# Kernel tuning notes

Hardware: AMD Instinct MI355X
Metric: run time of the kernel (lower is better)

## Reference

```python
import jax, jax.numpy as jnp
import numpy as np

K_MASK = -2.3819763e+38
B, T, D = 2, 2048, 2048
N, K, H = 8, 2, 256          # query heads, kv heads, head dim
F = 8192                     # ffn hidden
A = 4                        # num_altup_inputs
P = 4                        # num_modalities
WINDOW = 512
SOFT_CAP = 50.0
Q_SCALE = H ** -0.5
ROPE_BASE = 10000.0


def rms_norm(x, scale=None, eps=1e-6):
    y = x * jax.lax.rsqrt(jnp.mean(jnp.square(x), axis=-1, keepdims=True) + eps)
    if scale is not None:
        y = y * (1.0 + scale)   # scale_plus_one=True
    return y


def apply_rope(x, pos, base=ROPE_BASE, scale_factor=1.0):
    # x: [B,T,num_heads,H], pos: [B,T]
    h = x.shape[-1]
    frac = 2.0 * jnp.arange(h // 2, dtype=jnp.float32) / h
    timescale = base ** frac
    sin_inp = (pos[..., None].astype(jnp.float32) / timescale)[..., None, :] / scale_factor  # [B,T,1,H/2]
    sin, cos = jnp.sin(sin_inp), jnp.cos(sin_inp)
    x1, x2 = jnp.split(x, 2, axis=-1)
    return jnp.concatenate([x1 * cos - x2 * sin, x2 * cos + x1 * sin], axis=-1).astype(x.dtype)


def setup_inputs():
    key = jax.random.key(0)
    ks = jax.random.split(key, 12)
    r = lambda i, shape, s=0.02: jax.random.normal(ks[i], shape, dtype=jnp.float32) * s
    pos = jnp.broadcast_to(jnp.arange(T, dtype=jnp.int32), (B, T))
    causal = pos[:, :, None] >= pos[:, None, :]  # [B,T,T] bool
    return dict(
        x=jax.random.normal(ks[0], (A, B, T, D), dtype=jnp.float32),
        segment_pos=pos,
        attn_mask=causal,
        router_w=r(1, (D, P), 1.0),
        pred_coefs=r(2, (P, A, A), 0.0001),
        corr_coefs=r(3, (P, A), 0.01),
        correct_output_scale=jnp.ones((D,), jnp.float32),
        pre_attn_scale=jnp.zeros((D,), jnp.float32),
        q_w=r(4, (N, D, H)),
        kv_w=r(5, (2, K, D, H)),
        qk_q_scale=jnp.zeros((H,), jnp.float32),
        qk_k_scale=jnp.zeros((H,), jnp.float32),
        o_w=r(6, (N, H, D)),
        post_attn_scale=jnp.zeros((D,), jnp.float32),
        pre_ffw_scale=jnp.zeros((D,), jnp.float32),
        gate_w=r(7, (D, F)),
        up_w=r(8, (D, F)),
        down_w=r(9, (F, D)),
        post_ffw_scale=jnp.zeros((D,), jnp.float32),
    )


def _router(h, router_w):
    # modality router: scale by 1/d_model, project, tanh in fp32
    return jnp.tanh(jnp.einsum('btd,dp->btp', h * (1.0 / D), router_w).astype(jnp.float32))


def _attention(x, segment_pos, attn_mask, q_w, kv_w, qk_q_scale, qk_k_scale, o_w):
    q = jnp.einsum('btd,ndh->btnh', x, q_w)               # [B,T,N,H]
    k, v = jnp.einsum('bsd,ckdh->cbskh', x, kv_w)         # each [B,T,K,H]
    q = rms_norm(q, qk_q_scale)                           # qk norm
    k = rms_norm(k, qk_k_scale)
    v = rms_norm(v)                                       # value norm (no scale)
    q = apply_rope(q, segment_pos) * Q_SCALE
    k = apply_rope(k, segment_pos)
    g = N // K                                            # GQA group size
    qr = q.reshape(B, T, K, g, H)
    logits = jnp.einsum('btkgh,bskh->btkgs', qr, k).reshape(B, T, N, T)
    logits = jnp.tanh(logits / SOFT_CAP) * SOFT_CAP       # attn_logits_soft_cap
    # sliding-window mask combined with causal attn_mask
    sliding = (segment_pos[:, None, :] > segment_pos[:, :, None] - WINDOW) & \
              (segment_pos[:, None, :] < segment_pos[:, :, None] + WINDOW)
    mask = attn_mask & sliding
    padded = jnp.where(mask[:, :, None, :], logits, K_MASK)
    probs = jax.nn.softmax(padded, axis=-1).astype(k.dtype)
    enc = jnp.einsum('btkgs,bskh->btkgh', probs.reshape(B, T, K, g, T), v).reshape(B, T, N, H)
    return jnp.einsum('btnh,nhd->btd', enc, o_w)


def reference(x, segment_pos, attn_mask, router_w, pred_coefs, corr_coefs,
              correct_output_scale, pre_attn_scale, q_w, kv_w, qk_q_scale, qk_k_scale,
              o_w, post_attn_scale, pre_ffw_scale, gate_w, up_w, down_w, post_ffw_scale):
    # ---- AltUp predict ----
    mods = _router(x[0], router_w)                                   # [B,T,P]
    coefs = jnp.einsum('btp,pij->btij', mods, pred_coefs.astype(jnp.float32))
    predictions = x + jnp.einsum('btij,jbtd->ibtd', coefs, x).astype(x.dtype)
    active = predictions[0]
    # ---- attention block ----
    attn_in = rms_norm(active, pre_attn_scale)
    attn = _attention(attn_in, segment_pos, attn_mask, q_w, kv_w, qk_q_scale, qk_k_scale, o_w)
    attn = rms_norm(attn, post_attn_scale)
    attn_gated = active + attn
    # ---- gated-GELU MLP ----
    h = rms_norm(attn_gated, pre_ffw_scale)
    ffw = jnp.einsum('btf,fd->btd', jax.nn.gelu(h @ gate_w) * (h @ up_w), down_w)
    ffw = rms_norm(ffw, post_ffw_scale)
    activated = attn_gated + ffw
    # ---- AltUp correct (with scale_corrected_output) ----
    activated = activated * correct_output_scale
    mods_c = _router(activated, router_w)
    c = jnp.einsum('btp,pi->bti', mods_c, corr_coefs.astype(jnp.float32)) + 1.0
    innovation = activated - predictions[0]
    corrected = predictions + jnp.einsum('bti,btd->ibtd', c, innovation).astype(x.dtype)
    return corrected
```

## Files before the change

kernel.cpp:

```cpp
#include <hip/hip_runtime.h>
#include <hip/hip_bf16.h>

typedef unsigned short u16;
typedef __attribute__((ext_vector_type(8))) short bf16x8_t;
typedef __attribute__((ext_vector_type(4))) float f32x4_t;

#define DEV __device__ __forceinline__

constexpr int cB = 2, cT = 2048, cD = 2048;
constexpr int cN = 8, cK = 2, cH = 256, cF = 8192;
constexpr int cBT = cB * cT;
constexpr float cEPS = 1e-6f;
constexpr float cQS = 0.0625f;
constexpr float cCAP = 50.0f;
constexpr int cWIN = 512;
constexpr int cNH = 12;

DEV u16 f2bf(float f) {
  union { float f; unsigned u; } c; c.f = f;
  unsigned u = c.u;
  return (u16)((u + 0x7fffu + ((u >> 16) & 1u)) >> 16);
}
DEV float bf2f(u16 h) {
  union { unsigned u; float f; } c; c.u = ((unsigned)h) << 16;
  return c.f;
}
DEV float g4(const float4& v, int k) { return k == 0 ? v.x : k == 1 ? v.y : k == 2 ? v.z : v.w; }
DEV void store_bf4(u16* p, float a, float b, float c, float d) {
  union { u16 h[4]; uint2 v; } o;
  o.h[0] = f2bf(a); o.h[1] = f2bf(b); o.h[2] = f2bf(c); o.h[3] = f2bf(d);
  *(uint2*)p = o.v;
}
DEV float tanh_fast(float x) {
  float e2 = __expf(2.0f * x);
  return 1.0f - 2.0f * __builtin_amdgcn_rcpf(e2 + 1.0f);
}
DEV float gelu_fast(float x) {
  float u = 1.5957691216057308f * (x + 0.044715f * x * x * x);
  float e2 = __expf(u);
  return x * (1.0f - __builtin_amdgcn_rcpf(e2 + 1.0f));
}

DEV float block_sum256(float v, float* sbuf) {
  #pragma unroll
  for (int m = 32; m > 0; m >>= 1) v += __shfl_xor(v, m, 64);
  int wid = threadIdx.x >> 6;
  if ((threadIdx.x & 63) == 0) sbuf[wid] = v;
  __syncthreads();
  float tot = sbuf[0] + sbuf[1] + sbuf[2] + sbuf[3];
  __syncthreads();
  return tot;
}
DEV void block_sum256x4(float v[4], float* sbuf ) {
  #pragma unroll
  for (int m = 32; m > 0; m >>= 1) {
    #pragma unroll
    for (int k = 0; k < 4; k++) v[k] += __shfl_xor(v[k], m, 64);
  }
  int wid = threadIdx.x >> 6;
  if ((threadIdx.x & 63) == 0) *(float4*)(sbuf + wid * 4) = make_float4(v[0], v[1], v[2], v[3]);
  __syncthreads();
  #pragma unroll
  for (int k = 0; k < 4; k++) v[k] = sbuf[k] + sbuf[4 + k] + sbuf[8 + k] + sbuf[12 + k];
  __syncthreads();
}

#define GLD_LDS16(gp, lp) __builtin_amdgcn_global_load_lds( \
    (const __attribute__((address_space(1))) void*)(gp),    \
    (__attribute__((address_space(3))) void*)(lp), 16, 0, 0)

#define WAITV(n) asm volatile("s_waitcnt vmcnt(" #n ")" ::: "memory")
#define LGKM(n)  asm volatile("s_waitcnt lgkmcnt(" #n ")" ::: "memory")
#define SCHED0() __builtin_amdgcn_sched_barrier(0)
#define LDS_ADDR(p) ((unsigned)(uintptr_t)(__attribute__((address_space(3))) const void*)(p))
#define DSR(dst, base, off) \
  asm volatile("ds_read_b128 %0, %1 offset:" off : "=v"(dst) : "v"(base))

__global__ __launch_bounds__(256) void k_transpose_cast(
    const float* __restrict__ src, u16* __restrict__ dst, int R, int C, int gu) {
  __shared__ float tile[64][65];
  size_t base = (size_t)blockIdx.z * R * C;
  int c0 = blockIdx.x * 64, r0 = blockIdx.y * 64;
  int tx = threadIdx.x & 15, ty = threadIdx.x >> 4;
  #pragma unroll
  for (int i = 0; i < 4; i++) {
    int r = ty + i * 16;
    float4 v = *(const float4*)(src + base + (size_t)(r0 + r) * C + c0 + tx * 4);
    tile[r][tx * 4 + 0] = v.x; tile[r][tx * 4 + 1] = v.y;
    tile[r][tx * 4 + 2] = v.z; tile[r][tx * 4 + 3] = v.w;
  }
  __syncthreads();
  #pragma unroll
  for (int i = 0; i < 4; i++) {
    int j = ty + i * 16;
    int c = c0 + j;
    int n = (gu < 0) ? c : (((c >> 4) << 5) + (gu << 4) + (c & 15));
    store_bf4(dst + base + (size_t)n * R + r0 + tx * 4,
              tile[tx * 4 + 0][j], tile[tx * 4 + 1][j],
              tile[tx * 4 + 2][j], tile[tx * 4 + 3][j]);
  }
}

__global__ __launch_bounds__(256) void k_rope_table(
    const int* __restrict__ pos, float2* __restrict__ rt) {
  int idx = blockIdx.x * 256 + threadIdx.x;
  int bt = idx >> 7, j = idx & 127;
  float p = (float)pos[bt];
  float ts = powf(10000.0f, (2.0f * j) * (1.0f / cH));
  float si = p / ts;
  rt[idx] = make_float2(sinf(si), cosf(si));
}

__global__ __launch_bounds__(256) void k_predict(
    const float* __restrict__ x, const float* __restrict__ router_w,
    const float* __restrict__ pred_coefs, const float* __restrict__ pre_attn_scale,
    float* __restrict__ out, u16* __restrict__ attn_in) {
  __shared__ float sbuf[16];
  int bt = blockIdx.x, tid = threadIdx.x;
  const size_t PL = (size_t)cBT * cD;
  const size_t rowb = (size_t)bt * cD;
  float4 xv[4][2];
  #pragma unroll
  for (int j = 0; j < 4; j++)
    #pragma unroll
    for (int u = 0; u < 2; u++)
      xv[j][u] = *(const float4*)(x + j * PL + rowb + (u * 256 + tid) * 4);
  float rp[4] = {0, 0, 0, 0};
  #pragma unroll
  for (int u = 0; u < 2; u++)
    #pragma unroll
    for (int k = 0; k < 4; k++) {
      int e = (u * 256 + tid) * 4 + k;
      float4 rw = *(const float4*)(router_w + (size_t)e * 4);
      float xe = g4(xv[0][u], k);
      rp[0] += xe * rw.x; rp[1] += xe * rw.y; rp[2] += xe * rw.z; rp[3] += xe * rw.w;
    }
  block_sum256x4(rp, sbuf);
  float mods[4];
  #pragma unroll
  for (int p = 0; p < 4; p++) mods[p] = tanh_fast(rp[p] * (1.0f / cD));
  float coef[4][4];
  #pragma unroll
  for (int i = 0; i < 4; i++)
    #pragma unroll
    for (int j = 0; j < 4; j++) {
      float s = 0;
      #pragma unroll
      for (int p = 0; p < 4; p++) s += mods[p] * pred_coefs[(p * 4 + i) * 4 + j];
      coef[i][j] = s;
    }
  float4 p04[2]; float ssq = 0;
  #pragma unroll
  for (int u = 0; u < 2; u++)
    #pragma unroll
    for (int i = 0; i < 4; i++) {
      float4 s = xv[i][u];
      #pragma unroll
      for (int j = 0; j < 4; j++) {
        s.x += coef[i][j] * xv[j][u].x; s.y += coef[i][j] * xv[j][u].y;
        s.z += coef[i][j] * xv[j][u].z; s.w += coef[i][j] * xv[j][u].w;
      }
      *(float4*)(out + i * PL + rowb + (u * 256 + tid) * 4) = s;
      if (i == 0) { p04[u] = s; ssq += s.x * s.x + s.y * s.y + s.z * s.z + s.w * s.w; }
    }
  float rs = rsqrtf(block_sum256(ssq, sbuf) * (1.0f / cD) + cEPS);
  #pragma unroll
  for (int u = 0; u < 2; u++) {
    int e0 = (u * 256 + tid) * 4;
    float4 sc = *(const float4*)(pre_attn_scale + e0);
    store_bf4(attn_in + rowb + e0,
              p04[u].x * rs * (1.0f + sc.x), p04[u].y * rs * (1.0f + sc.y),
              p04[u].z * rs * (1.0f + sc.z), p04[u].w * rs * (1.0f + sc.w));
  }
}

template <int OUT_MODE>
__global__ __launch_bounds__(512, 2) void k_gemm8p(
    const u16* __restrict__ A, const u16* __restrict__ Bt, void* __restrict__ Cv,
    int Nn, int Kk) {
  constexpr int MI = 8;
  constexpr int A_KS = 256 * 32;
  constexpr int B_KS = 256 * 32;
  constexpr int BUF_E = 2 * A_KS + 2 * B_KS;
  extern __shared__ u16 lds[];

  const int tid = threadIdx.x;
  const int wid = tid >> 6, lane = tid & 63;
  const int wr = wid >> 2, wc = wid & 3;
  const int fr = lane & 15, fq = lane >> 4;

  const int nwg = gridDim.x * gridDim.y;
  const int flat = blockIdx.y * gridDim.x + blockIdx.x;
  const int swz = (flat & 7) * (nwg >> 3) + (flat >> 3);
  const int m0 = (swz % gridDim.x) * 256;
  const int n0 = (swz / gridDim.x) * 256;
  const int NT = Kk >> 6;
  const int NH = NT * 2;

  const int srow = lane >> 2, sslot = lane & 3;
  const int scol = (sslot ^ ((srow >> 1) & 3)) * 8;
  const u16* aSrc0 = A + (size_t)(m0 + wid * 16 + srow) * Kk + scol;
  const u16* aSrc1 = A + (size_t)(m0 + 128 + wid * 16 + srow) * Kk + scol;
  const u16* bSrc0 = Bt + (size_t)(n0 + wid * 16 + srow) * Kk + scol;
  const u16* bSrc1 = Bt + (size_t)(n0 + 128 + wid * 16 + srow) * Kk + scol;

  const int swzR = (fq ^ ((fr >> 1) & 3)) * 8;
  const unsigned base0 = LDS_ADDR(lds);
  const unsigned aoffB = (unsigned)(((wr * 128 + fr) * 32 + swzR) * 2);
  const unsigned boffB = (unsigned)((2 * A_KS + (wc * 64 + fr) * 32 + swzR) * 2);
  const unsigned aB0 = base0 + aoffB, aB1 = base0 + BUF_E * 2 + aoffB;
  const unsigned bB0 = base0 + boffB, bB1 = base0 + BUF_E * 2 + boffB;

  auto stageH = [&](int h) {
    int tt = h >> 1, ks = h & 1;
    int koff = h * 32;
    u16* dstA = lds + (tt & 1) * BUF_E + ks * A_KS + wid * 512;
    GLD_LDS16(aSrc0 + koff, dstA);
    GLD_LDS16(aSrc1 + koff, dstA + 128 * 32);
    u16* dstB = lds + (tt & 1) * BUF_E + 2 * A_KS + ks * B_KS + wid * 512;
    GLD_LDS16(bSrc0 + koff, dstB);
    GLD_LDS16(bSrc1 + koff, dstB + 128 * 32);
  };

  f32x4_t acc[MI][4];
  #pragma unroll
  for (int i = 0; i < MI; i++)
    #pragma unroll
    for (int j = 0; j < 4; j++) acc[i][j] = (f32x4_t){0.f, 0.f, 0.f, 0.f};

  bf16x8_t aX[8], aY[8], bX[4], bY[4];

#define READS_KS0(ab, bb, av, bv) do {                                   \
    DSR(av[0], ab, "0");     DSR(av[1], ab, "1024");                     \
    DSR(av[2], ab, "2048");  DSR(av[3], ab, "3072");                     \
    DSR(av[4], ab, "4096");  DSR(av[5], ab, "5120");                     \
    DSR(av[6], ab, "6144");  DSR(av[7], ab, "7168");                     \
    DSR(bv[0], bb, "0");     DSR(bv[1], bb, "1024");                     \
    DSR(bv[2], bb, "2048");  DSR(bv[3], bb, "3072");  } while (0)
#define READS_KS1(ab, bb, av, bv) do {                                   \
    DSR(av[0], ab, "16384"); DSR(av[1], ab, "17408");                    \
    DSR(av[2], ab, "18432"); DSR(av[3], ab, "19456");                    \
    DSR(av[4], ab, "20480"); DSR(av[5], ab, "21504");                    \
    DSR(av[6], ab, "22528"); DSR(av[7], ab, "23552");                    \
    DSR(bv[0], bb, "16384"); DSR(bv[1], bb, "17408");                    \
    DSR(bv[2], bb, "18432"); DSR(bv[3], bb, "19456"); } while (0)

#define MFMA32(av, bv)                                                    \
  __builtin_amdgcn_s_setprio(1);                                          \
  _Pragma("unroll")                                                       \
  for (int i = 0; i < 8; i++) {                                           \
    acc[i][0] = __builtin_amdgcn_mfma_f32_16x16x32_bf16(av[i], bv[0], acc[i][0], 0, 0, 0); \
    acc[i][1] = __builtin_amdgcn_mfma_f32_16x16x32_bf16(av[i], bv[1], acc[i][1], 0, 0, 0); \
    acc[i][2] = __builtin_amdgcn_mfma_f32_16x16x32_bf16(av[i], bv[2], acc[i][2], 0, 0, 0); \
    acc[i][3] = __builtin_amdgcn_mfma_f32_16x16x32_bf16(av[i], bv[3], acc[i][3], 0, 0, 0); \
  }                                                                       \
  __builtin_amdgcn_s_setprio(0);

  stageH(0); asm volatile("" ::: "memory");
  stageH(1); asm volatile("" ::: "memory");
  stageH(2);
  WAITV(8);
  __builtin_amdgcn_s_barrier();
  SCHED0();
  READS_KS0(aB0, bB0, aX, bX);

  for (int t = 0; t < NT; t++) {
    const unsigned aPb = (t & 1) ? aB1 : aB0;
    const unsigned bPb = (t & 1) ? bB1 : bB0;
    const unsigned aNb = (t & 1) ? aB0 : aB1;
    const unsigned bNb = (t & 1) ? bB0 : bB1;

    {
      const int R = NH - 1 - 2 * t;
      if (R >= 2) WAITV(4); else WAITV(0);
      __builtin_amdgcn_s_barrier();
      SCHED0();
      if (R >= 3) stageH(2 * t + 3);
      READS_KS1(aPb, bPb, aY, bY);
      LGKM(12);
      SCHED0();
      MFMA32(aX, bX)
    }
    {
      const int R = NH - 2 - 2 * t;
      if (R >= 2) WAITV(4); else if (R == 1) WAITV(0);
      __builtin_amdgcn_s_barrier();
      SCHED0();
      if (R >= 3) stageH(2 * t + 4);
      if (R >= 1) {
        READS_KS0(aNb, bNb, aX, bX);
        LGKM(12);
      } else {
        LGKM(0);
      }
      SCHED0();
      MFMA32(aY, bY)
    }
  }
#undef MFMA32
#undef READS_KS0
#undef READS_KS1

  if constexpr (OUT_MODE == 2) {
    const int Nh = Nn >> 1;
    #pragma unroll
    for (int i = 0; i < MI; i++)
      #pragma unroll
      for (int jp = 0; jp < 2; jp++) {
        int c = (n0 + wc * 64 + jp * 32) / 2 + fr;
        #pragma unroll
        for (int r = 0; r < 4; r++) {
          int m = m0 + wr * (MI * 16) + i * 16 + fq * 4 + r;
          float g = acc[i][2 * jp][r], uu = acc[i][2 * jp + 1][r];
          ((u16*)Cv)[(size_t)m * Nh + c] = f2bf(gelu_fast(g) * uu);
        }
      }
  } else {
    #pragma unroll
    for (int i = 0; i < MI; i++)
      #pragma unroll
      for (int j = 0; j < 4; j++)
        #pragma unroll
        for (int r = 0; r < 4; r++) {
          int m = m0 + wr * (MI * 16) + i * 16 + fq * 4 + r;
          int n = n0 + wc * 64 + j * 16 + fr;
          ((u16*)Cv)[(size_t)m * Nn + n] = f2bf(acc[i][j][r]);
        }
  }
}

template <int OUT_MODE>
__global__ __launch_bounds__(512, 2) void k_gemm4r(
    const u16* __restrict__ A, const u16* __restrict__ Bt, void* __restrict__ Cv,
    int Nn, int Kk) {
  constexpr int MI = 4;
  constexpr int BM = 128;
  constexpr int A_KS = BM * 32;
  constexpr int B_KS = 256 * 32;
  constexpr int SLOT_E = 2 * A_KS + 2 * B_KS;
  extern __shared__ u16 lds[];

  const int tid = threadIdx.x;
  const int wid = tid >> 6, lane = tid & 63;
  const int wr = wid >> 2, wc = wid & 3;
  const int fr = lane & 15, fq = lane >> 4;

  const int nwg = gridDim.x * gridDim.y;
  const int flat = blockIdx.y * gridDim.x + blockIdx.x;
  const int swz = (flat & 7) * (nwg >> 3) + (flat >> 3);
  const int m0 = (swz % gridDim.x) * BM;
  const int n0 = (swz / gridDim.x) * 256;
  const int NT = Kk >> 6;

  const int srow = lane >> 2, sslot = lane & 3;

  auto stageA = [&](int t, int ks) {
    u16* buf = lds + (t % 3) * SLOT_E + ks * A_KS;
    int row0 = wid * 16;
    int row = row0 + srow;
    int col = (sslot ^ ((row >> 1) & 3)) * 8;
    GLD_LDS16(A + (size_t)(m0 + row) * Kk + t * 64 + ks * 32 + col, buf + row0 * 32);
  };
  auto stageB = [&](int t, int ks) {
    u16* buf = lds + (t % 3) * SLOT_E + 2 * A_KS + ks * B_KS;
    #pragma unroll
    for (int i = 0; i < 2; i++) {
      int row0 = i * 128 + wid * 16;
      int row = row0 + srow;
      int col = (sslot ^ ((row >> 1) & 3)) * 8;
      GLD_LDS16(Bt + (size_t)(n0 + row) * Kk + t * 64 + ks * 32 + col, buf + row0 * 32);
    }
  };
  auto readA = [&](const u16* buf, int ks, int i) -> bf16x8_t {
    int row = wr * 64 + i * 16 + fr;
    return *(const bf16x8_t*)(buf + ks * A_KS + row * 32 + (fq ^ ((row >> 1) & 3)) * 8);
  };
  auto readB = [&](const u16* buf, int ks, int j) -> bf16x8_t {
    int row = wc * 64 + j * 16 + fr;
    return *(const bf16x8_t*)(buf + 2 * A_KS + ks * B_KS + row * 32 + (fq ^ ((row >> 1) & 3)) * 8);
  };

  f32x4_t acc[MI][4];
  #pragma unroll
  for (int i = 0; i < MI; i++)
    #pragma unroll
    for (int j = 0; j < 4; j++) acc[i][j] = (f32x4_t){0.f, 0.f, 0.f, 0.f};

  stageA(0, 0); stageB(0, 0); stageA(0, 1); stageB(0, 1);
  stageA(1, 0); stageB(1, 0); stageA(1, 1); stageB(1, 1);
  WAITV(9);
  __builtin_amdgcn_s_barrier();

#define PHASE_MFMA4(J0)                                                             \
  __builtin_amdgcn_s_setprio(1);                                                    \
  _Pragma("unroll")                                                                 \
  for (int i = 0; i < MI; i++) {                                                    \
    acc[i][J0]     = __builtin_amdgcn_mfma_f32_16x16x32_bf16(a0[i], b0[0], acc[i][J0], 0, 0, 0);     \
    acc[i][J0 + 1] = __builtin_amdgcn_mfma_f32_16x16x32_bf16(a0[i], b0[1], acc[i][J0 + 1], 0, 0, 0); \
  }                                                                                 \
  __builtin_amdgcn_s_setprio(0);

  for (int t = 0; t < NT; t++) {
    const u16* buf = lds + (t % 3) * SLOT_E;
    const bool pf2 = (t + 2 < NT);
    const bool pf1 = (t + 1 < NT);
    bf16x8_t a0[MI], b0[2];

    #pragma unroll
    for (int i = 0; i < MI; i++) a0[i] = readA(buf, 0, i);
    b0[0] = readB(buf, 0, 0); b0[1] = readB(buf, 0, 1);
    if (pf2) stageA(t + 2, 0);
    __builtin_amdgcn_s_barrier();
    PHASE_MFMA4(0)
    __builtin_amdgcn_s_barrier();

    b0[0] = readB(buf, 0, 2); b0[1] = readB(buf, 0, 3);
    if (pf2) stageB(t + 2, 0);
    if (pf2) WAITV(9); else if (pf1) WAITV(6); else WAITV(0);
    __builtin_amdgcn_s_barrier();
    PHASE_MFMA4(2)
    __builtin_amdgcn_s_barrier();

    #pragma unroll
    for (int i = 0; i < MI; i++) a0[i] = readA(buf, 1, i);
    b0[0] = readB(buf, 1, 0); b0[1] = readB(buf, 1, 1);
    if (pf2) stageA(t + 2, 1);
    __builtin_amdgcn_s_barrier();
    PHASE_MFMA4(0)
    __builtin_amdgcn_s_barrier();

    b0[0] = readB(buf, 1, 2); b0[1] = readB(buf, 1, 3);
    if (pf2) stageB(t + 2, 1);
    if (pf2) WAITV(9); else if (pf1) WAITV(3);
    __builtin_amdgcn_s_barrier();
    PHASE_MFMA4(2)
    __builtin_amdgcn_s_barrier();
  }
#undef PHASE_MFMA4

  #pragma unroll
  for (int i = 0; i < MI; i++)
    #pragma unroll
    for (int j = 0; j < 4; j++)
      #pragma unroll
      for (int r = 0; r < 4; r++) {
        int m = m0 + wr * 64 + i * 16 + fq * 4 + r;
        int n = n0 + wc * 64 + j * 16 + fr;
        float v = acc[i][j][r];
        if (OUT_MODE == 1) ((u16*)Cv)[(size_t)m * Nn + n] = f2bf(v);
        else ((float*)Cv)[(size_t)m * Nn + n] = v;
      }
}

__global__ __launch_bounds__(64) void k_qkvpost(
    u16* __restrict__ qkv, const float* __restrict__ qscale,
    const float* __restrict__ kscale, const float2* __restrict__ rt,
    u16* __restrict__ vT) {
  int h = blockIdx.x % cNH, bt = blockIdx.x / cNH;
  int lane = threadIdx.x;
  u16* row = qkv + ((size_t)bt * cNH + h) * cH;
  float v[4], ssq = 0;
  #pragma unroll
  for (int m = 0; m < 4; m++) { v[m] = bf2f(row[lane + 64 * m]); ssq += v[m] * v[m]; }
  #pragma unroll
  for (int mm = 32; mm > 0; mm >>= 1) ssq += __shfl_xor(ssq, mm, 64);
  float rs = rsqrtf(ssq * (1.0f / cH) + cEPS);
  if (h < 10) {
    const float* sc = (h < 8) ? qscale : kscale;
    float os = (h < 8) ? cQS : 1.0f;
    #pragma unroll
    for (int m = 0; m < 4; m++) {
      int e = lane + 64 * m;
      v[m] = v[m] * rs * (1.0f + sc[e]);
    }
    #pragma unroll
    for (int m = 0; m < 2; m++) {
      int j = lane + 64 * m;
      float2 t = rt[bt * 128 + j];
      float x1 = v[m], x2 = v[m + 2];
      row[j]       = f2bf((x1 * t.y - x2 * t.x) * os);
      row[j + 128] = f2bf((x2 * t.y + x1 * t.x) * os);
    }
  } else {
    int kk = h - 10;
    int b = bt / cT, t = bt % cT;
    #pragma unroll
    for (int m = 0; m < 4; m++) {
      int e = lane + 64 * m;
      vT[((size_t)(b * cK + kk) * cH + e) * cT + t] = f2bf(v[m] * rs);
    }
  }
}

__global__ __launch_bounds__(64) void k_attn(
    const u16* __restrict__ qkv, const u16* __restrict__ vT, u16* __restrict__ enc) {
  int t0 = blockIdx.x * 16;
  int n = blockIdx.y, b = blockIdx.z;
  int kn = n >> 2;
  int lane = threadIdx.x;
  int fr = lane & 15, fq = lane >> 4;
  __shared__ float P[16][33];

  bf16x8_t qf[8];
  const u16* qrow = qkv + ((size_t)(b * cT + t0 + fr) * cNH + n) * cH;
  #pragma unroll
  for (int ks = 0; ks < 8; ks++) qf[ks] = *(const bf16x8_t*)(qrow + ks * 32 + fq * 8);

  f32x4_t acc[16];
  #pragma unroll
  for (int ht = 0; ht < 16; ht++) acc[ht] = (f32x4_t){0.f, 0.f, 0.f, 0.f};
  float psum[4] = {0.f, 0.f, 0.f, 0.f};

  int s_lo = t0 - (cWIN - 1); if (s_lo < 0) s_lo = 0; s_lo &= ~31;
  for (int s0 = s_lo; s0 <= t0 + 15; s0 += 32) {
    f32x4_t S[2];
    S[0] = (f32x4_t){0.f, 0.f, 0.f, 0.f};
    S[1] = (f32x4_t){0.f, 0.f, 0.f, 0.f};
    #pragma unroll
    for (int c = 0; c < 2; c++) {
      const u16* krow = qkv + ((size_t)(b * cT + s0 + c * 16 + fr) * cNH + 8 + kn) * cH;
      #pragma unroll
      for (int ks = 0; ks < 8; ks++) {
        bf16x8_t kf = *(const bf16x8_t*)(krow + ks * 32 + fq * 8);
        S[c] = __builtin_amdgcn_mfma_f32_16x16x32_bf16(qf[ks], kf, S[c], 0, 0, 0);
      }
    }
    #pragma unroll
    for (int c = 0; c < 2; c++) {
      int s = s0 + c * 16 + fr;
      #pragma unroll
      for (int r = 0; r < 4; r++) {
        int t = t0 + fq * 4 + r;
        float l = cCAP * tanh_fast(S[c][r] * (1.0f / cCAP));
        float pe = (s <= t && s >= t - (cWIN - 1)) ? __expf(l) : 0.0f;
        psum[r] += pe;
        P[fq * 4 + r][c * 16 + fr] = pe;
      }
    }
    bf16x8_t pf;
    #pragma unroll
    for (int e = 0; e < 8; e++) pf[e] = (short)f2bf(P[fr][fq * 8 + e]);
    #pragma unroll
    for (int ht = 0; ht < 16; ht++) {
      bf16x8_t vf = *(const bf16x8_t*)(vT + (((size_t)(b * cK + kn)) * cH + ht * 16 + fr) * cT + s0 + fq * 8);
      acc[ht] = __builtin_amdgcn_mfma_f32_16x16x32_bf16(pf, vf, acc[ht], 0, 0, 0);
    }
  }
  #pragma unroll
  for (int r = 0; r < 4; r++) {
    #pragma unroll
    for (int m = 1; m < 16; m <<= 1) psum[r] += __shfl_xor(psum[r], m, 64);
  }
  float inv[4];
  #pragma unroll
  for (int r = 0; r < 4; r++) inv[r] = 1.0f / psum[r];
  #pragma unroll
  for (int ht = 0; ht < 16; ht++)
    #pragma unroll
    for (int r = 0; r < 4; r++)
      enc[(((size_t)(b * cT + t0 + fq * 4 + r)) * cN + n) * cH + ht * 16 + fr] =
          f2bf(acc[ht][r] * inv[r]);
}

__global__ __launch_bounds__(256) void k_postattn(
    const float* __restrict__ attn_raw, const float* __restrict__ out0,
    const float* __restrict__ post_attn_scale, const float* __restrict__ pre_ffw_scale,
    float* __restrict__ ag, u16* __restrict__ h) {
  __shared__ float sbuf[4];
  int bt = blockIdx.x, tid = threadIdx.x;
  const size_t rowb = (size_t)bt * cD;
  float4 ar[2]; float ssq = 0;
  #pragma unroll
  for (int u = 0; u < 2; u++) {
    ar[u] = *(const float4*)(attn_raw + rowb + (u * 256 + tid) * 4);
    ssq += ar[u].x * ar[u].x + ar[u].y * ar[u].y + ar[u].z * ar[u].z + ar[u].w * ar[u].w;
  }
  float rs = rsqrtf(block_sum256(ssq, sbuf) * (1.0f / cD) + cEPS);
  float4 agv[2]; float ssq2 = 0;
  #pragma unroll
  for (int u = 0; u < 2; u++) {
    int e0 = (u * 256 + tid) * 4;
    float4 o0 = *(const float4*)(out0 + rowb + e0);
    float4 sc = *(const float4*)(post_attn_scale + e0);
    float4 a;
    a.x = o0.x + ar[u].x * rs * (1.0f + sc.x);
    a.y = o0.y + ar[u].y * rs * (1.0f + sc.y);
    a.z = o0.z + ar[u].z * rs * (1.0f + sc.z);
    a.w = o0.w + ar[u].w * rs * (1.0f + sc.w);
    agv[u] = a;
    *(float4*)(ag + rowb + e0) = a;
    ssq2 += a.x * a.x + a.y * a.y + a.z * a.z + a.w * a.w;
  }
  float rs2 = rsqrtf(block_sum256(ssq2, sbuf) * (1.0f / cD) + cEPS);
  #pragma unroll
  for (int u = 0; u < 2; u++) {
    int e0 = (u * 256 + tid) * 4;
    float4 sc = *(const float4*)(pre_ffw_scale + e0);
    store_bf4(h + rowb + e0,
              agv[u].x * rs2 * (1.0f + sc.x), agv[u].y * rs2 * (1.0f + sc.y),
              agv[u].z * rs2 * (1.0f + sc.z), agv[u].w * rs2 * (1.0f + sc.w));
  }
}

__global__ __launch_bounds__(256) void k_final(
    const float* __restrict__ ffw_raw, const float* __restrict__ ag,
    const float* __restrict__ post_ffw_scale, const float* __restrict__ cos_scale,
    const float* __restrict__ router_w, const float* __restrict__ corr_coefs,
    float* __restrict__ out) {
  __shared__ float sbuf[16];
  int bt = blockIdx.x, tid = threadIdx.x;
  const size_t PL = (size_t)cBT * cD;
  const size_t rowb = (size_t)bt * cD;
  float4 fv[2]; float ssq = 0;
  #pragma unroll
  for (int u = 0; u < 2; u++) {
    fv[u] = *(const float4*)(ffw_raw + rowb + (u * 256 + tid) * 4);
    ssq += fv[u].x * fv[u].x + fv[u].y * fv[u].y + fv[u].z * fv[u].z + fv[u].w * fv[u].w;
  }
  float rs = rsqrtf(block_sum256(ssq, sbuf) * (1.0f / cD) + cEPS);
  float4 av[2];
  float rp[4] = {0, 0, 0, 0};
  #pragma unroll
  for (int u = 0; u < 2; u++) {
    int e0 = (u * 256 + tid) * 4;
    float4 agx = *(const float4*)(ag + rowb + e0);
    float4 ps = *(const float4*)(post_ffw_scale + e0);
    float4 cs = *(const float4*)(cos_scale + e0);
    float4 a;
    a.x = (agx.x + fv[u].x * rs * (1.0f + ps.x)) * cs.x;
    a.y = (agx.y + fv[u].y * rs * (1.0f + ps.y)) * cs.y;
    a.z = (agx.z + fv[u].z * rs * (1.0f + ps.z)) * cs.z;
    a.w = (agx.w + fv[u].w * rs * (1.0f + ps.w)) * cs.w;
    av[u] = a;
    #pragma unroll
    for (int k = 0; k < 4; k++) {
      float4 rw = *(const float4*)(router_w + (size_t)(e0 + k) * 4);
      float xe = g4(a, k);
      rp[0] += xe * rw.x; rp[1] += xe * rw.y; rp[2] += xe * rw.z; rp[3] += xe * rw.w;
    }
  }
  block_sum256x4(rp, sbuf);
  float cc[4];
  #pragma unroll
  for (int i = 0; i < 4; i++) {
    float s = 1.0f;
    #pragma unroll
    for (int p = 0; p < 4; p++) s += tanh_fast(rp[p] * (1.0f / cD)) * corr_coefs[p * 4 + i];
    cc[i] = s;
  }
  #pragma unroll
  for (int u = 0; u < 2; u++) {
    size_t o = rowb + (u * 256 + tid) * 4;
    float4 p0 = *(const float4*)(out + o);
    float4 in4;
    in4.x = av[u].x - p0.x; in4.y = av[u].y - p0.y;
    in4.z = av[u].z - p0.z; in4.w = av[u].w - p0.w;
    float4 w0;
    w0.x = p0.x + cc[0] * in4.x; w0.y = p0.y + cc[0] * in4.y;
    w0.z = p0.z + cc[0] * in4.z; w0.w = p0.w + cc[0] * in4.w;
    *(float4*)(out + o) = w0;
    #pragma unroll
    for (int i = 1; i < 4; i++) {
      float4 q = *(const float4*)(out + i * PL + o);
      q.x += cc[i] * in4.x; q.y += cc[i] * in4.y;
      q.z += cc[i] * in4.z; q.w += cc[i] * in4.w;
      *(float4*)(out + i * PL + o) = q;
    }
  }
}

extern "C" void kernel_launch(void* const* d_in, const int* in_sizes, int n_in,
                              void* d_out, int out_size, void* d_ws, size_t ws_size,
                              hipStream_t stream) {
  const float* x              = (const float*)d_in[0];
  const int*   pos            = (const int*)d_in[1];
  const float* router_w       = (const float*)d_in[3];
  const float* pred_coefs     = (const float*)d_in[4];
  const float* corr_coefs     = (const float*)d_in[5];
  const float* cos_scale      = (const float*)d_in[6];
  const float* pre_attn_scale = (const float*)d_in[7];
  const float* q_w            = (const float*)d_in[8];
  const float* kv_w           = (const float*)d_in[9];
  const float* qk_q_scale     = (const float*)d_in[10];
  const float* qk_k_scale     = (const float*)d_in[11];
  const float* o_w            = (const float*)d_in[12];
  const float* post_attn_scale= (const float*)d_in[13];
  const float* pre_ffw_scale  = (const float*)d_in[14];
  const float* gate_w         = (const float*)d_in[15];
  const float* up_w           = (const float*)d_in[16];
  const float* down_w         = (const float*)d_in[17];
  const float* post_ffw_scale = (const float*)d_in[18];
  float* out = (float*)d_out;

  char* wsp = (char*)d_ws;
  size_t off = 0;
  auto take = [&](size_t nbytes) -> char* {
    char* p = wsp + off;
    off += (nbytes + 255) & ~((size_t)255);
    return p;
  };
  u16* gu_wT    = (u16*)take((size_t)2 * cF * cD * 2);
  u16* down_wT  = (u16*)take((size_t)cD * cF * 2);
  u16* qkv_wT   = (u16*)take((size_t)cNH * cH * cD * 2);
  u16* o_wT     = (u16*)take((size_t)cD * cN * cH * 2);
  u16* attn_in  = (u16*)take((size_t)cBT * cD * 2);
  u16* qkvbuf   = (u16*)take((size_t)cBT * cNH * cH * 2);
  u16* vTbuf    = (u16*)take((size_t)cB * cK * cH * cT * 2);
  u16* encbuf   = (u16*)take((size_t)cBT * cN * cH * 2);
  float* attn_raw = (float*)take((size_t)cBT * cD * 4);
  float* agbuf    = (float*)take((size_t)cBT * cD * 4);
  u16* hbuf     = (u16*)take((size_t)cBT * cD * 2);
  u16* Gcbuf    = (u16*)take((size_t)cBT * cF * 2);
  float* ffw_raw = (float*)take((size_t)cBT * cD * 4);
  float2* ropetab = (float2*)take((size_t)cBT * 128 * 8);
  (void)in_sizes; (void)n_in; (void)out_size; (void)ws_size;

  dim3 blk256(256), blk64(64), blk512(512);
  constexpr unsigned LDS8  = 2 * (2 * 256 * 32 + 2 * 256 * 32) * 2;
  constexpr unsigned LDS4R = 3 * (2 * 128 * 32 + 2 * 256 * 32) * 2;

  k_transpose_cast<<<dim3(cF / 64, cD / 64, 1), blk256, 0, stream>>>(gate_w, gu_wT, cD, cF, 0);
  k_transpose_cast<<<dim3(cF / 64, cD / 64, 1), blk256, 0, stream>>>(up_w, gu_wT, cD, cF, 1);
  k_transpose_cast<<<dim3(cD / 64, cF / 64, 1), blk256, 0, stream>>>(down_w, down_wT, cF, cD, -1);
  k_transpose_cast<<<dim3(cH / 64, cD / 64, cN), blk256, 0, stream>>>(q_w, qkv_wT, cD, cH, -1);
  k_transpose_cast<<<dim3(cH / 64, cD / 64, 2 * cK), blk256, 0, stream>>>(
      kv_w, qkv_wT + (size_t)cN * cH * cD, cD, cH, -1);
  k_transpose_cast<<<dim3(cD / 64, (cN * cH) / 64, 1), blk256, 0, stream>>>(o_w, o_wT, cN * cH, cD, -1);
  k_rope_table<<<dim3(cBT * 128 / 256), blk256, 0, stream>>>(pos, ropetab);

  k_predict<<<dim3(cBT), blk256, 0, stream>>>(x, router_w, pred_coefs, pre_attn_scale, out, attn_in);

  k_gemm4r<1><<<dim3(cBT / 128, (cNH * cH) / 256), blk512, LDS4R, stream>>>(
      attn_in, qkv_wT, qkvbuf, cNH * cH, cD);

  k_qkvpost<<<dim3(cBT * cNH), blk64, 0, stream>>>(qkvbuf, qk_q_scale, qk_k_scale, ropetab, vTbuf);

  k_attn<<<dim3(cT / 16, cN, cB), blk64, 0, stream>>>(qkvbuf, vTbuf, encbuf);

  k_gemm4r<0><<<dim3(cBT / 128, cD / 256), blk512, LDS4R, stream>>>(
      encbuf, o_wT, attn_raw, cD, cN * cH);
  k_postattn<<<dim3(cBT), blk256, 0, stream>>>(attn_raw, out, post_attn_scale, pre_ffw_scale, agbuf, hbuf);

  k_gemm8p<2><<<dim3(cBT / 256, (2 * cF) / 256), blk512, LDS8, stream>>>(
      hbuf, gu_wT, Gcbuf, 2 * cF, cD);
  k_gemm4r<0><<<dim3(cBT / 128, cD / 256), blk512, LDS4R, stream>>>(
      Gcbuf, down_wT, ffw_raw, cD, cF);

  k_final<<<dim3(cBT), blk256, 0, stream>>>(ffw_raw, agbuf, post_ffw_scale, cos_scale,
                                            router_w, corr_coefs, out);
}
```

Baseline: 950.5 us.

## Rewrite 128x256 GEMM main loop with double-buffered register prefetch and inline-asm LDS reads

Replaces the k_gemm4r main loop with a restructured k_gemm4p. It prefetches the next half-K slice of A/B fragments from LDS into a second register set (aX/aY, bX/bY) while MFMAs run on the current set. LDS reads now use precomputed byte addresses with immediate offsets via inline asm, and barriers per K-tile drop from eight to two. The aim is to hide LDS latency behind MFMA work and cut address arithmetic and synchronisation, at the cost of more VGPRs and reliance on hand-placed waitcnt and scheduling barriers.

```diff
diff --git a/kernel.cpp b/kernel.cpp
--- a/kernel.cpp
+++ b/kernel.cpp
@@ -330,14 +330,13 @@
 }
 
 template <int OUT_MODE>
-__global__ __launch_bounds__(512, 2) void k_gemm4r(
+__global__ __launch_bounds__(512, 2) void k_gemm4p(
     const u16* __restrict__ A, const u16* __restrict__ Bt, void* __restrict__ Cv,
     int Nn, int Kk) {
-  constexpr int MI = 4;
-  constexpr int BM = 128;
-  constexpr int A_KS = BM * 32;
+  constexpr int A_KS = 128 * 32;
   constexpr int B_KS = 256 * 32;
   constexpr int SLOT_E = 2 * A_KS + 2 * B_KS;
+  constexpr unsigned SLOT_B = 49152;
   extern __shared__ u16 lds[];
 
   const int tid = threadIdx.x;
@@ -348,98 +347,115 @@
   const int nwg = gridDim.x * gridDim.y;
   const int flat = blockIdx.y * gridDim.x + blockIdx.x;
   const int swz = (flat & 7) * (nwg >> 3) + (flat >> 3);
-  const int m0 = (swz % gridDim.x) * BM;
+  const int m0 = (swz % gridDim.x) * 128;
   const int n0 = (swz / gridDim.x) * 256;
   const int NT = Kk >> 6;
+  const int NH = NT * 2;
 
   const int srow = lane >> 2, sslot = lane & 3;
-
-  auto stageA = [&](int t, int ks) {
-    u16* buf = lds + (t % 3) * SLOT_E + ks * A_KS;
-    int row0 = wid * 16;
-    int row = row0 + srow;
-    int col = (sslot ^ ((row >> 1) & 3)) * 8;
-    GLD_LDS16(A + (size_t)(m0 + row) * Kk + t * 64 + ks * 32 + col, buf + row0 * 32);
+  const int scol = (sslot ^ ((srow >> 1) & 3)) * 8;
+  const u16* aSrc  = A + (size_t)(m0 + wid * 16 + srow) * Kk + scol;
+  const u16* bSrc0 = Bt + (size_t)(n0 + wid * 16 + srow) * Kk + scol;
+  const u16* bSrc1 = Bt + (size_t)(n0 + 128 + wid * 16 + srow) * Kk + scol;
+
+  const int swzR = (fq ^ ((fr >> 1) & 3)) * 8;
+  const unsigned base0 = LDS_ADDR(lds);
+  const unsigned aoffB = (unsigned)(((wr * 64 + fr) * 32 + swzR) * 2);
+  const unsigned boffB = (unsigned)((2 * A_KS + (wc * 64 + fr) * 32 + swzR) * 2);
+  const unsigned aS0 = base0 + aoffB;
+  const unsigned bS0 = base0 + boffB;
+  const unsigned aLast = aS0 + 2 * SLOT_B, bLast = bS0 + 2 * SLOT_B;
+
+  unsigned aCur = aS0, bCur = bS0;
+  unsigned aNxt = aS0 + SLOT_B, bNxt = bS0 + SLOT_B;
+
+  auto stageH = [&](int h) {
+    int tt = h >> 1, ks = h & 1;
+    int slot = tt % 3;
+    int koff = h * 32;
+    u16* dstA = lds + slot * SLOT_E + ks * A_KS + wid * 512;
+    GLD_LDS16(aSrc + koff, dstA);
+    u16* dstB = lds + slot * SLOT_E + 2 * A_KS + ks * B_KS + wid * 512;
+    GLD_LDS16(bSrc0 + koff, dstB);
+    GLD_LDS16(bSrc1 + koff, dstB + 128 * 32);
   };
-  auto stageB = [&](int t, int ks) {
-    u16* buf = lds + (t % 3) * SLOT_E + 2 * A_KS + ks * B_KS;
-    #pragma unroll
-    for (int i = 0; i < 2; i++) {
-      int row0 = i * 128 + wid * 16;
-      int row = row0 + srow;
-      int col = (sslot ^ ((row >> 1) & 3)) * 8;
-      GLD_LDS16(Bt + (size_t)(n0 + row) * Kk + t * 64 + ks * 32 + col, buf + row0 * 32);
-    }
-  };
-  auto readA = [&](const u16* buf, int ks, int i) -> bf16x8_t {
-    int row = wr * 64 + i * 16 + fr;
-    return *(const bf16x8_t*)(buf + ks * A_KS + row * 32 + (fq ^ ((row >> 1) & 3)) * 8);
-  };
-  auto readB = [&](const u16* buf, int ks, int j) -> bf16x8_t {
-    int row = wc * 64 + j * 16 + fr;
-    return *(const bf16x8_t*)(buf + 2 * A_KS + ks * B_KS + row * 32 + (fq ^ ((row >> 1) & 3)) * 8);
-  };
-
-  f32x4_t acc[MI][4];
-  #pragma unroll
-  for (int i = 0; i < MI; i++)
+
+  f32x4_t acc[4][4];
+  #pragma unroll
+  for (int i = 0; i < 4; i++)
     #pragma unroll
     for (int j = 0; j < 4; j++) acc[i][j] = (f32x4_t){0.f, 0.f, 0.f, 0.f};
 
-  stageA(0, 0); stageB(0, 0); stageA(0, 1); stageB(0, 1);
-  stageA(1, 0); stageB(1, 0); stageA(1, 1); stageB(1, 1);
+  bf16x8_t aX[4], aY[4], bX[4], bY[4];
+
+#define R4_KS0(ab, bb, av, bv) do {                                      \
+    DSR(av[0], ab, "0");     DSR(av[1], ab, "1024");                     \
+    DSR(av[2], ab, "2048");  DSR(av[3], ab, "3072");                     \
+    DSR(bv[0], bb, "0");     DSR(bv[1], bb, "1024");                     \
+    DSR(bv[2], bb, "2048");  DSR(bv[3], bb, "3072");  } while (0)
+#define R4_KS1(ab, bb, av, bv) do {                                      \
+    DSR(av[0], ab, "8192");  DSR(av[1], ab, "9216");                     \
+    DSR(av[2], ab, "10240"); DSR(av[3], ab, "11264");                    \
+    DSR(bv[0], bb, "16384"); DSR(bv[1], bb, "17408");                    \
+    DSR(bv[2], bb, "18432"); DSR(bv[3], bb, "19456"); } while (0)
+
+#define MFMA16(av, bv)                                                    \
+  __builtin_amdgcn_s_setprio(1);                                          \
+  _Pragma("unroll")                                                       \
+  for (int i = 0; i < 4; i++) {                                           \
+    acc[i][0] = __builtin_amdgcn_mfma_f32_16x16x32_bf16(av[i], bv[0], acc[i][0], 0, 0, 0); \
+    acc[i][1] = __builtin_amdgcn_mfma_f32_16x16x32_bf16(av[i], bv[1], acc[i][1], 0, 0, 0); \
+    acc[i][2] = __builtin_amdgcn_mfma_f32_16x16x32_bf16(av[i], bv[2], acc[i][2], 0, 0, 0); \
+    acc[i][3] = __builtin_amdgcn_mfma_f32_16x16x32_bf16(av[i], bv[3], acc[i][3], 0, 0, 0); \
+  }                                                                       \
+  __builtin_amdgcn_s_setprio(0);
+
+  stageH(0); asm volatile("" ::: "memory");
+  stageH(1); asm volatile("" ::: "memory");
+  stageH(2); asm volatile("" ::: "memory");
+  stageH(3);
   WAITV(9);
   __builtin_amdgcn_s_barrier();
-
-#define PHASE_MFMA4(J0)                                                             \
-  __builtin_amdgcn_s_setprio(1);                                                    \
-  _Pragma("unroll")                                                                 \
-  for (int i = 0; i < MI; i++) {                                                    \
-    acc[i][J0]     = __builtin_amdgcn_mfma_f32_16x16x32_bf16(a0[i], b0[0], acc[i][J0], 0, 0, 0);     \
-    acc[i][J0 + 1] = __builtin_amdgcn_mfma_f32_16x16x32_bf16(a0[i], b0[1], acc[i][J0 + 1], 0, 0, 0); \
-  }                                                                                 \
-  __builtin_amdgcn_s_setprio(0);
+  SCHED0();
+  R4_KS0(aCur, bCur, aX, bX);
 
   for (int t = 0; t < NT; t++) {
-    const u16* buf = lds + (t % 3) * SLOT_E;
-    const bool pf2 = (t + 2 < NT);
-    const bool pf1 = (t + 1 < NT);
-    bf16x8_t a0[MI], b0[2];
-
-    #pragma unroll
-    for (int i = 0; i < MI; i++) a0[i] = readA(buf, 0, i);
-    b0[0] = readB(buf, 0, 0); b0[1] = readB(buf, 0, 1);
-    if (pf2) stageA(t + 2, 0);
-    __builtin_amdgcn_s_barrier();
-    PHASE_MFMA4(0)
-    __builtin_amdgcn_s_barrier();
-
-    b0[0] = readB(buf, 0, 2); b0[1] = readB(buf, 0, 3);
-    if (pf2) stageB(t + 2, 0);
-    if (pf2) WAITV(9); else if (pf1) WAITV(6); else WAITV(0);
-    __builtin_amdgcn_s_barrier();
-    PHASE_MFMA4(2)
-    __builtin_amdgcn_s_barrier();
-
-    #pragma unroll
-    for (int i = 0; i < MI; i++) a0[i] = readA(buf, 1, i);
-    b0[0] = readB(buf, 1, 0); b0[1] = readB(buf, 1, 1);
-    if (pf2) stageA(t + 2, 1);
-    __builtin_amdgcn_s_barrier();
-    PHASE_MFMA4(0)
-    __builtin_amdgcn_s_barrier();
-
-    b0[0] = readB(buf, 1, 2); b0[1] = readB(buf, 1, 3);
-    if (pf2) stageB(t + 2, 1);
-    if (pf2) WAITV(9); else if (pf1) WAITV(3);
-    __builtin_amdgcn_s_barrier();
-    PHASE_MFMA4(2)
-    __builtin_amdgcn_s_barrier();
-  }
-#undef PHASE_MFMA4
-
-  #pragma unroll
-  for (int i = 0; i < MI; i++)
+    {
+      const int R = NH - 1 - 2 * t;
+      if (R >= 3) WAITV(6); else WAITV(0);
+      __builtin_amdgcn_s_barrier();
+      SCHED0();
+      if (R >= 4) stageH(2 * t + 4);
+      R4_KS1(aCur, bCur, aY, bY);
+      LGKM(8);
+      SCHED0();
+      MFMA16(aX, bX)
+    }
+    {
+      const int R = NH - 2 - 2 * t;
+      if (R >= 3) WAITV(6); else if (R == 2) WAITV(3); else if (R == 1) WAITV(0);
+      __builtin_amdgcn_s_barrier();
+      SCHED0();
+      if (R >= 4) stageH(2 * t + 5);
+      if (R >= 1) {
+        R4_KS0(aNxt, bNxt, aX, bX);
+        LGKM(8);
+      } else {
+        LGKM(0);
+      }
+      SCHED0();
+      MFMA16(aY, bY)
+    }
+    aCur = aNxt; bCur = bNxt;
+    aNxt = (aNxt == aLast) ? aS0 : aNxt + SLOT_B;
+    bNxt = (bNxt == bLast) ? bS0 : bNxt + SLOT_B;
+  }
+#undef MFMA16
+#undef R4_KS0
+#undef R4_KS1
+
+  #pragma unroll
+  for (int i = 0; i < 4; i++)
     #pragma unroll
     for (int j = 0; j < 4; j++)
       #pragma unroll
@@ -730,20 +746,20 @@
 
   k_predict<<<dim3(cBT), blk256, 0, stream>>>(x, router_w, pred_coefs, pre_attn_scale, out, attn_in);
 
-  k_gemm4r<1><<<dim3(cBT / 128, (cNH * cH) / 256), blk512, LDS4R, stream>>>(
+  k_gemm4p<1><<<dim3(cBT / 128, (cNH * cH) / 256), blk512, LDS4R, stream>>>(
       attn_in, qkv_wT, qkvbuf, cNH * cH, cD);
 
   k_qkvpost<<<dim3(cBT * cNH), blk64, 0, stream>>>(qkvbuf, qk_q_scale, qk_k_scale, ropetab, vTbuf);
 
   k_attn<<<dim3(cT / 16, cN, cB), blk64, 0, stream>>>(qkvbuf, vTbuf, encbuf);
 
-  k_gemm4r<0><<<dim3(cBT / 128, cD / 256), blk512, LDS4R, stream>>>(
+  k_gemm4p<0><<<dim3(cBT / 128, cD / 256), blk512, LDS4R, stream>>>(
       encbuf, o_wT, attn_raw, cD, cN * cH);
   k_postattn<<<dim3(cBT), blk256, 0, stream>>>(attn_raw, out, post_attn_scale, pre_ffw_scale, agbuf, hbuf);
 
   k_gemm8p<2><<<dim3(cBT / 256, (2 * cF) / 256), blk512, LDS8, stream>>>(
       hbuf, gu_wT, Gcbuf, 2 * cF, cD);
-  k_gemm4r<0><<<dim3(cBT / 128, cD / 256), blk512, LDS4R, stream>>>(
+  k_gemm4p<0><<<dim3(cBT / 128, cD / 256), blk512, LDS4R, stream>>>(
       Gcbuf, down_wT, ffw_raw, cD, cF);
 
   k_final<<<dim3(cBT), blk256, 0, stream>>>(ffw_raw, agbuf, post_ffw_scale, cos_scale,
```

Result: no change. 933.8 us (-1.8%).
